# Kernel tuning notes

Measured on AMD Instinct MI355X. Metric: run time of the kernel, lower is better.

Reference implementation:

```python
import jax, jax.numpy as jnp
import numpy as np

N, C, H_IMG, W_IMG = 32, 3, 224, 224
P = 14                      # number_patches per side
PH, PW = H_IMG // P, W_IMG // P
IN_DIM = C * PH * PW        # 768
D = 768                     # hidden_dimension
NH = 12                     # number_heads
DH = D // NH                # 64
L = 12                      # number_blocks
OUT = 1000                  # output_dimension
S = P * P + 1               # 197 tokens (cls + patches)
MLP = 4 * D                 # mlp_ratio * d


def sinusoidal_pos_emb(s, d):
    # result[i][j] = sin(i / 10000^(j/d)) if j even else cos(i / 10000^((j-1)/d))
    i = np.arange(s, dtype=np.float64)[:, None]
    j = np.arange(d)[None, :]
    angle = i / (10000.0 ** ((j - (j % 2)) / float(d)))
    emb = np.where(j % 2 == 0, np.sin(angle), np.cos(angle))
    return jnp.asarray(emb, jnp.float32)


def setup_inputs() -> dict:
    key = jax.random.key(0)
    ks = jax.random.split(key, 12)
    f32 = jnp.float32
    p = {}
    p['images'] = jax.random.normal(ks[0], (N, C, H_IMG, W_IMG), f32)
    p['W_map'] = jax.random.normal(ks[1], (IN_DIM, D), f32) * 0.02
    p['b_map'] = jnp.zeros((D,), f32)
    p['class_token'] = jax.random.normal(ks[2], (1, D), f32)
    p['pos_emb'] = sinusoidal_pos_emb(S, D)  # frozen (requires_grad=False)
    p['ln1_g'] = jnp.ones((L, D), f32)
    p['ln1_b'] = jnp.zeros((L, D), f32)
    p['Wq'] = jax.random.normal(ks[3], (L, NH, DH, DH), f32) * 0.02
    p['bq'] = jnp.zeros((L, NH, DH), f32)
    p['Wk'] = jax.random.normal(ks[4], (L, NH, DH, DH), f32) * 0.02
    p['bk'] = jnp.zeros((L, NH, DH), f32)
    p['Wv'] = jax.random.normal(ks[5], (L, NH, DH, DH), f32) * 0.02
    p['bv'] = jnp.zeros((L, NH, DH), f32)
    p['ln2_g'] = jnp.ones((L, D), f32)
    p['ln2_b'] = jnp.zeros((L, D), f32)
    p['W1'] = jax.random.normal(ks[6], (L, D, MLP), f32) * 0.02
    p['b1'] = jnp.zeros((L, MLP), f32)
    p['W2'] = jax.random.normal(ks[7], (L, MLP, D), f32) * 0.02
    p['b2'] = jnp.zeros((L, D), f32)
    p['W_head'] = jax.random.normal(ks[8], (D, OUT), f32) * 0.02
    p['b_head'] = jnp.zeros((OUT,), f32)
    return p


def _layer_norm(x, g, b, eps=1e-5):
    mu = jnp.mean(x, axis=-1, keepdims=True)
    var = jnp.var(x, axis=-1, keepdims=True)
    return (x - mu) * jax.lax.rsqrt(var + eps) * g + b


def reference(images, W_map, b_map, class_token, pos_emb, ln1_g, ln1_b,
              Wq, bq, Wk, bk, Wv, bv, ln2_g, ln2_b, W1, b1, W2, b2,
              W_head, b_head):
    n = images.shape[0]
    # patchify: [N,C,H,W] -> [N, P*P, C*ph*pw]; per-patch flatten is (C,ph,pw) order
    patches = images.reshape(n, C, P, PH, P, PW)
    patches = patches.transpose(0, 2, 4, 1, 3, 5).reshape(n, P * P, IN_DIM)
    tokens = patches @ W_map + b_map                         # [N, P*P, D]
    cls = jnp.broadcast_to(class_token[None], (n, 1, D))
    x = jnp.concatenate([cls, tokens], axis=1) + pos_emb     # [N, S, D]

    scale = DH ** 0.5
    for l in range(L):
        # --- MHSA with per-head independent Linear weights ---
        h = _layer_norm(x, ln1_g[l], ln1_b[l])
        xh = h.reshape(n, S, NH, DH)
        q = jnp.einsum('nshd,hde->nshe', xh, Wq[l]) + bq[l]
        k = jnp.einsum('nshd,hde->nshe', xh, Wk[l]) + bk[l]
        v = jnp.einsum('nshd,hde->nshe', xh, Wv[l]) + bv[l]
        scores = jnp.einsum('nqhd,nkhd->nhqk', q, k) / scale  # [N,H,S,S]
        attn = jax.nn.softmax(scores, axis=-1)
        o = jnp.einsum('nhqk,nkhd->nqhd', attn, v).reshape(n, S, D)
        x = x + o
        # --- MLP (exact GELU, as torch.nn.GELU default) ---
        h2 = _layer_norm(x, ln2_g[l], ln2_b[l])
        m = jax.nn.gelu(h2 @ W1[l] + b1[l], approximate=False) @ W2[l] + b2[l]
        x = x + m

    logits = x[:, 0] @ W_head + b_head
    return jax.nn.softmax(logits, axis=-1)
```

## Files before the change

kernel.cpp:

```cpp
#include <hip/hip_runtime.h>
#include <hip/hip_bf16.h>

constexpr int N_   = 32;
constexpr int C_   = 3;
constexpr int P_   = 14;
constexpr int PHW  = 16;
constexpr int IND  = 768;
constexpr int D_   = 768;
constexpr int NH_  = 12;
constexpr int DH_  = 64;
constexpr int L_   = 12;
constexpr int OUT_ = 1000;
constexpr int S_   = 197;
constexpr int MLP_ = 3072;
constexpr int NPATCH = P_ * P_;
constexpr int ROWS   = N_ * S_;
constexpr int TROWS  = N_ * NPATCH;
constexpr int RPAD   = 6400;
constexpr int SP_R   = 256;
constexpr int SP_C   = 224;

typedef __attribute__((ext_vector_type(8))) short bf16x8;
typedef __attribute__((ext_vector_type(4))) float f32x4;

__device__ __forceinline__ float bf2f(ushort u) {
    union { float f; unsigned int i; } v; v.i = ((unsigned int)u) << 16; return v.f;
}
__device__ __forceinline__ ushort f2bf(float f) {
    union { float f; unsigned int i; } v; v.f = f;
    unsigned int r = v.i + 0x7fffu + ((v.i >> 16) & 1u);
    return (ushort)(r >> 16);
}

__global__ __launch_bounds__(256)
void mfma_gemm(const ushort* __restrict__ Ag,
               const ushort* __restrict__ Bg,
               void* __restrict__ Cg,
               const float* __restrict__ biasg,
               int M, int N, int K,
               int lda, int ldb, int ldc,
               long offA1, long offA2,
               long offB1, long offB2,
               long offC1, long offC2,
               long offS1, long offS2,
               int inner, float alpha, int act, int outbf, int accum,
               int swz, ushort* __restrict__ vtout, int splitK)
{
    const int bz = blockIdx.z;
    const int bi = bz / inner, bj = bz % inner;
    const ushort* A = Ag + bi * offA1 + bj * offA2;
    const ushort* B = Bg + bi * offB1 + bj * offB2;
    const long coff = bi * offC1 + bj * offC2;
    const float* bias = biasg ? (biasg + bi * offS1 + bj * offS2) : nullptr;

    int bx = blockIdx.x, by = blockIdx.y;
    if (swz) {
        const int gx = gridDim.x;
        const int nwg = gx * gridDim.y;
        const int orig = by * gx + bx;
        const int q = nwg >> 3, r = nwg & 7;
        const int xcd = orig & 7, loc = orig >> 3;
        const int wgid = (xcd < r ? xcd * (q + 1) : r * (q + 1) + (xcd - r) * q) + loc;
        bx = wgid % gx;
        by = wgid / gx;
    }

    __shared__ ushort As[2][128 * 32];
    __shared__ ushort Bs[2][128 * 32];

    const int tid  = threadIdx.x;
    const int w    = tid >> 6;
    const int lhi  = (tid & 63) >> 4;
    const int llo  = tid & 15;
    const int wr   = w >> 1, wc = w & 1;
    const int row0 = by * 128;
    const int col0 = bx * 128;

    f32x4 acc[4][4];
#pragma unroll
    for (int m = 0; m < 4; ++m)
#pragma unroll
        for (int n = 0; n < 4; ++n) acc[m][n] = (f32x4){0.f, 0.f, 0.f, 0.f};

    const int r0s = tid >> 2,        s0s = tid & 3;
    const int r1s = 64 + (tid >> 2), s1s = tid & 3;
    const int ss0 = s0s ^ ((r0s >> 1) & 3);
    const int ss1 = s1s ^ ((r1s >> 1) & 3);
    const int dst0 = (w << 6) << 3;
    const int dst1 = (256 + (w << 6)) << 3;

    const long arow0 = (long)(row0 + r0s) * lda + ss0 * 8;
    const long arow1 = (long)(row0 + r1s) * lda + ss1 * 8;
    const long brow0 = (long)(col0 + r0s) * ldb + ss0 * 8;
    const long brow1 = (long)(col0 + r1s) * ldb + ss1 * 8;

    const int kperblk = K / splitK;
    const int kbase   = (splitK > 1) ? bi * kperblk : 0;

#define STAGE(buf, k0)                                                                     \
    do {                                                                                   \
        __builtin_amdgcn_global_load_lds(                                                  \
            (const __attribute__((address_space(1))) void*)(A + arow0 + (k0)),             \
            (__attribute__((address_space(3))) void*)(&As[buf][0] + dst0), 16, 0, 0);      \
        __builtin_amdgcn_global_load_lds(                                                  \
            (const __attribute__((address_space(1))) void*)(A + arow1 + (k0)),             \
            (__attribute__((address_space(3))) void*)(&As[buf][0] + dst1), 16, 0, 0);      \
        __builtin_amdgcn_global_load_lds(                                                  \
            (const __attribute__((address_space(1))) void*)(B + brow0 + (k0)),             \
            (__attribute__((address_space(3))) void*)(&Bs[buf][0] + dst0), 16, 0, 0);      \
        __builtin_amdgcn_global_load_lds(                                                  \
            (const __attribute__((address_space(1))) void*)(B + brow1 + (k0)),             \
            (__attribute__((address_space(3))) void*)(&Bs[buf][0] + dst1), 16, 0, 0);      \
    } while (0)

    const int nt = kperblk >> 5;
    STAGE(0, kbase);
    for (int t = 0; t < nt; ++t) {
        const int cur = t & 1;
        if (t + 1 < nt) {
            STAGE(cur ^ 1, kbase + ((t + 1) << 5));
            asm volatile("s_waitcnt vmcnt(4)" ::: "memory");
        } else {
            asm volatile("s_waitcnt vmcnt(0)" ::: "memory");
        }
        __builtin_amdgcn_s_barrier();
        asm volatile("" ::: "memory");

        bf16x8 av[4], bv[4];
#pragma unroll
        for (int m = 0; m < 4; ++m) {
            int R = wr * 64 + m * 16 + llo;
            av[m] = *(const bf16x8*)(&As[cur][0] + R * 32 + ((lhi ^ ((R >> 1) & 3)) << 3));
        }
#pragma unroll
        for (int n = 0; n < 4; ++n) {
            int R = wc * 64 + n * 16 + llo;
            bv[n] = *(const bf16x8*)(&Bs[cur][0] + R * 32 + ((lhi ^ ((R >> 1) & 3)) << 3));
        }
#pragma unroll
        for (int m = 0; m < 4; ++m)
#pragma unroll
            for (int n = 0; n < 4; ++n)
                acc[m][n] = __builtin_amdgcn_mfma_f32_16x16x32_bf16(av[m], bv[n], acc[m][n], 0, 0, 0);

        asm volatile("" ::: "memory");
        __builtin_amdgcn_s_barrier();
    }
#undef STAGE

    float* Cf = (float*)Cg + coff;
    ushort* Ch = (ushort*)Cg + coff;
    const bool vpath = (vtout != nullptr) && (bi == 2);
#pragma unroll
    for (int m = 0; m < 4; ++m) {
#pragma unroll
        for (int n = 0; n < 4; ++n) {
#pragma unroll
            for (int j = 0; j < 4; ++j) {
                int gr = row0 + wr * 64 + m * 16 + lhi * 4 + j;
                int gc = col0 + wc * 64 + n * 16 + llo;
                if (gr >= M || gc >= N) continue;
                float v = acc[m][n][j] * alpha;
                if (splitK > 1) {
                    if (bias && bi == 0) v += bias[gc];
                    unsafeAtomicAdd(&Cf[(long)gr * ldc + gc], v);
                    continue;
                }
                if (bias) v += bias[gc];
                if (act == 1) v = 0.5f * v * (1.f + erff(v * 0.70710678118654752f));
                if (vpath) {
                    int nn = gr / 197, s = gr - nn * 197;
                    vtout[(((long)nn * NH_ + bj) * 64 + gc) * SP_C + s] = f2bf(v);
                } else {
                    long ci = (long)gr * ldc + gc;
                    if (outbf) {
                        Ch[ci] = f2bf(v);
                    } else {
                        if (accum) v += Cf[ci];
                        Cf[ci] = v;
                    }
                }
            }
        }
    }
}

__global__ __launch_bounds__(256)
void im2col_kernel(const float* __restrict__ img, ushort* __restrict__ patches)
{
    long idx = (long)blockIdx.x * 256 + threadIdx.x;
    if (idx >= (long)TROWS * IND) return;
    int e = (int)(idx % IND);
    int t = (int)((idx / IND) % NPATCH);
    int n = (int)(idx / ((long)IND * NPATCH));
    int pw = e & 15, ph = (e >> 4) & 15, c = e >> 8;
    int px = t % P_, py = t / P_;
    patches[idx] = f2bf(img[(((long)n * C_ + c) * 224 + py * PHW + ph) * 224 + px * PHW + pw]);
}

__global__ __launch_bounds__(256)
void assemble_kernel(const float* __restrict__ tokens,
                     const float* __restrict__ cls,
                     const float* __restrict__ pos,
                     float* __restrict__ x)
{
    long idx = (long)blockIdx.x * 256 + threadIdx.x;
    if (idx >= (long)ROWS * D_) return;
    int d = (int)(idx % D_);
    int s = (int)((idx / D_) % S_);
    long n = idx / ((long)D_ * S_);
    float v = (s == 0) ? cls[d] : tokens[((long)n * NPATCH + (s - 1)) * D_ + d];
    x[idx] = v + pos[(long)s * D_ + d];
}

__global__ __launch_bounds__(256)
void layernorm_kernel(const float* __restrict__ x, ushort* __restrict__ out,
                      const float* __restrict__ g, const float* __restrict__ b)
{
    long row = blockIdx.x;
    const float* xr = x + row * D_;
    ushort* orow = out + row * D_;
    int tid = threadIdx.x;
    float v0 = xr[tid], v1 = xr[tid + 256], v2 = xr[tid + 512];
    float s  = v0 + v1 + v2;
    float sq = v0 * v0 + v1 * v1 + v2 * v2;
    for (int off = 32; off > 0; off >>= 1) {
        s  += __shfl_down(s, off);
        sq += __shfl_down(sq, off);
    }
    __shared__ float rs[4], rq[4];
    int wave = tid >> 6, lane = tid & 63;
    if (lane == 0) { rs[wave] = s; rq[wave] = sq; }
    __syncthreads();
    float S  = rs[0] + rs[1] + rs[2] + rs[3];
    float SQ = rq[0] + rq[1] + rq[2] + rq[3];
    float mean = S * (1.f / 768.f);
    float var  = SQ * (1.f / 768.f) - mean * mean;
    float rstd = rsqrtf(var + 1e-5f);
    orow[tid]       = f2bf((v0 - mean) * rstd * g[tid]       + b[tid]);
    orow[tid + 256] = f2bf((v1 - mean) * rstd * g[tid + 256] + b[tid + 256]);
    orow[tid + 512] = f2bf((v2 - mean) * rstd * g[tid + 512] + b[tid + 512]);
}

__global__ __launch_bounds__(256)
void softmax197_kernel(ushort* __restrict__ scores)
{
    long rid = (long)blockIdx.x * 4 + (threadIdx.x >> 6);
    if (rid >= (long)N_ * NH_ * S_) return;
    long batch = rid / S_;
    long r = rid % S_;
    ushort* p = scores + (batch * SP_R + r) * SP_C;
    int lane = threadIdx.x & 63;
    float v[4];
    float mx = -INFINITY;
#pragma unroll
    for (int i = 0; i < 4; ++i) {
        int idx = lane + i * 64;
        v[i] = (idx < S_) ? bf2f(p[idx]) : -INFINITY;
        mx = fmaxf(mx, v[i]);
    }
    for (int off = 32; off > 0; off >>= 1) mx = fmaxf(mx, __shfl_xor(mx, off));
    float sum = 0.f;
#pragma unroll
    for (int i = 0; i < 4; ++i) {
        int idx = lane + i * 64;
        if (idx < S_) { v[i] = expf(v[i] - mx); sum += v[i]; }
    }
    for (int off = 32; off > 0; off >>= 1) sum += __shfl_xor(sum, off);
    float inv = 1.f / sum;
#pragma unroll
    for (int i = 0; i < 4; ++i) {
        int idx = lane + i * 64;
        if (idx < SP_C) p[idx] = (idx < S_) ? f2bf(v[i] * inv) : (ushort)0;
    }
}

__global__ __launch_bounds__(256)
void transcast_kernel(const float* __restrict__ in, ushort* __restrict__ out,
                      int R, int C, long inL, long outL)
{
    const float* ip = in + (long)blockIdx.z * inL;
    ushort* op = out + (long)blockIdx.z * outL;
    __shared__ float t[32][33];
    int c0 = blockIdx.x * 32, r0 = blockIdx.y * 32;
    int tx = threadIdx.x & 31, ty = threadIdx.x >> 5;
#pragma unroll
    for (int i = 0; i < 4; ++i) {
        int r = r0 + ty * 4 + i, c = c0 + tx;
        float v = 0.f;
        if (r < R && c < C) v = ip[(long)r * C + c];
        t[ty * 4 + i][tx] = v;
    }
    __syncthreads();
#pragma unroll
    for (int i = 0; i < 4; ++i) {
        int c = c0 + ty * 4 + i, r = r0 + tx;
        if (c < C && r < R) op[(long)c * R + r] = f2bf(t[tx][ty * 4 + i]);
    }
}

__global__ __launch_bounds__(256)
void transf32_kernel(const float* __restrict__ in, float* __restrict__ out, int R, int C)
{
    __shared__ float t[32][33];
    int c0 = blockIdx.x * 32, r0 = blockIdx.y * 32;
    int tx = threadIdx.x & 31, ty = threadIdx.x >> 5;
#pragma unroll
    for (int i = 0; i < 4; ++i) {
        int r = r0 + ty * 4 + i, c = c0 + tx;
        float v = 0.f;
        if (r < R && c < C) v = in[(long)r * C + c];
        t[ty * 4 + i][tx] = v;
    }
    __syncthreads();
#pragma unroll
    for (int i = 0; i < 4; ++i) {
        int c = c0 + ty * 4 + i, r = r0 + tx;
        if (c < C && r < R) out[(long)c * R + r] = t[tx][ty * 4 + i];
    }
}

__global__ __launch_bounds__(256)
void build_wqkvC_kernel(const float* __restrict__ Wq, const float* __restrict__ Wk,
                        const float* __restrict__ Wv, int l0, ushort* __restrict__ out)
{
    long idx = (long)blockIdx.x * 256 + threadIdx.x;
    if (idx >= 36L * 4096) return;
    int z = blockIdx.z, l = l0 + z;
    int sec = (int)(idx / 49152);
    int r   = (int)(idx % 49152);
    int h = r / 4096, rr = r % 4096, e = rr / 64, d = rr % 64;
    const float* W = sec == 0 ? Wq : (sec == 1 ? Wk : Wv);
    out[(long)z * 147456 + idx] = f2bf(W[(((long)l * NH_ + h) * 64 + d) * 64 + e]);
}

__global__ __launch_bounds__(256)
void build_bqkv_kernel(const float* __restrict__ bq, const float* __restrict__ bk,
                       const float* __restrict__ bv, float* __restrict__ out)
{
    int i = blockIdx.x * 256 + threadIdx.x;
    if (i >= L_ * 2304) return;
    int l = i / 2304, n = i % 2304;
    int sec = n / 768, h = (n % 768) / 64, e = n % 64;
    const float* b = sec == 0 ? bq : (sec == 1 ? bk : bv);
    out[i] = b[((long)l * NH_ + h) * 64 + e];
}

__global__ __launch_bounds__(256)
void head_kernel(const float* __restrict__ x, const float* __restrict__ Wt,
                 const float* __restrict__ bhead, float* __restrict__ logits)
{
    int wid = blockIdx.x * 4 + (threadIdx.x >> 6);
    int lane = threadIdx.x & 63;
    int n = wid / OUT_, c = wid % OUT_;
    if (n >= N_) return;
    const float* xr = x + (long)n * S_ * D_;
    const float* wr = Wt + (long)c * D_;
    float acc = 0.f;
#pragma unroll
    for (int i = 0; i < 12; ++i) acc += xr[lane + i * 64] * wr[lane + i * 64];
    for (int off = 32; off > 0; off >>= 1) acc += __shfl_down(acc, off);
    if (lane == 0) logits[(long)n * OUT_ + c] = acc + bhead[c];
}

__global__ __launch_bounds__(256)
void softmax_out_kernel(const float* __restrict__ logits, float* __restrict__ out)
{
    int row = blockIdx.x;
    int tid = threadIdx.x;
    const float* p = logits + (long)row * OUT_;
    float v[4];
    float mx = -INFINITY;
#pragma unroll
    for (int i = 0; i < 4; ++i) {
        int idx = tid + i * 256;
        v[i] = (idx < OUT_) ? p[idx] : -INFINITY;
        mx = fmaxf(mx, v[i]);
    }
    int wave = tid >> 6, lane = tid & 63;
    for (int off = 32; off > 0; off >>= 1) mx = fmaxf(mx, __shfl_xor(mx, off));
    __shared__ float r1[4], r2[4];
    if (lane == 0) r1[wave] = mx;
    __syncthreads();
    mx = fmaxf(fmaxf(r1[0], r1[1]), fmaxf(r1[2], r1[3]));
    float sum = 0.f;
#pragma unroll
    for (int i = 0; i < 4; ++i) {
        int idx = tid + i * 256;
        if (idx < OUT_) { v[i] = expf(v[i] - mx); sum += v[i]; }
    }
    for (int off = 32; off > 0; off >>= 1) sum += __shfl_xor(sum, off);
    if (lane == 0) r2[wave] = sum;
    __syncthreads();
    sum = r2[0] + r2[1] + r2[2] + r2[3];
    float inv = 1.f / sum;
#pragma unroll
    for (int i = 0; i < 4; ++i) {
        int idx = tid + i * 256;
        if (idx < OUT_) out[(long)row * OUT_ + idx] = v[i] * inv;
    }
}

extern "C" void kernel_launch(void* const* d_in, const int* in_sizes, int n_in,
                              void* d_out, int out_size, void* d_ws, size_t ws_size,
                              hipStream_t stream)
{
    const float* images = (const float*)d_in[0];
    const float* W_map  = (const float*)d_in[1];
    const float* b_map  = (const float*)d_in[2];
    const float* cls    = (const float*)d_in[3];
    const float* pos    = (const float*)d_in[4];
    const float* ln1_g  = (const float*)d_in[5];
    const float* ln1_b  = (const float*)d_in[6];
    const float* Wq     = (const float*)d_in[7];
    const float* bq     = (const float*)d_in[8];
    const float* Wk     = (const float*)d_in[9];
    const float* bk     = (const float*)d_in[10];
    const float* Wv     = (const float*)d_in[11];
    const float* bv     = (const float*)d_in[12];
    const float* ln2_g  = (const float*)d_in[13];
    const float* ln2_b  = (const float*)d_in[14];
    const float* W1     = (const float*)d_in[15];
    const float* b1     = (const float*)d_in[16];
    const float* W2     = (const float*)d_in[17];
    const float* b2     = (const float*)d_in[18];
    const float* W_head = (const float*)d_in[19];
    const float* b_head = (const float*)d_in[20];

    char* base = (char*)d_ws;
    float*  x       = (float*)base;   base += 19660800L;
    ushort* hbuf    = (ushort*)base;  base += 9830400L;
    ushort* qkv     = (ushort*)base;  base += 29491200L;
    ushort* Vt      = (ushort*)base;  base += 11038720L;
    ushort* scoresP = (ushort*)base;  base += 44040192L;
    ushort* mbuf    = (ushort*)base;  base += 39321600L;
    ushort* Wmapt   = (ushort*)base;  base += 1179648L;
    float*  bqkvA   = (float*)base;   base += 110592L;
    ushort* WqkvC   = (ushort*)base;  base += 3538944L;

    size_t used = (size_t)(base - (char*)d_ws);
    const long W1L_ALL = 56623104L, W2L_ALL = 56623104L;
    const long W1L_ONE = 4718592L,  W2L_ONE = 4718592L;
    bool hoist = ws_size >= used + (size_t)(W1L_ALL + W2L_ALL);
    ushort* W1tA = (ushort*)base;  base += hoist ? W1L_ALL : W1L_ONE;
    ushort* W2tA = (ushort*)base;  base += hoist ? W2L_ALL : W2L_ONE;
    const long w1str = hoist ? 3072L * 768 : 0;
    const long w2str = hoist ? 768L * 3072 : 0;

    float* W_headT = (float*)scoresP;
    float* logits  = (float*)((char*)scoresP + 3072000L);
    float*  tokens  = (float*)scoresP;
    ushort* patches = mbuf;

    build_wqkvC_kernel<<<dim3(576, 1, L_), 256, 0, stream>>>(Wq, Wk, Wv, 0, WqkvC);
    build_bqkv_kernel<<<(L_ * 2304 + 255) / 256, 256, 0, stream>>>(bq, bk, bv, bqkvA);
    transcast_kernel<<<dim3(24, 24, 1), 256, 0, stream>>>(W_map, Wmapt, IND, D_, 0L, 0L);
    if (hoist) {
        transcast_kernel<<<dim3(96, 24, L_), 256, 0, stream>>>(W1, W1tA, D_, MLP_,
                                                               (long)D_ * MLP_, 3072L * 768);
        transcast_kernel<<<dim3(24, 96, L_), 256, 0, stream>>>(W2, W2tA, MLP_, D_,
                                                               (long)MLP_ * D_, 768L * 3072);
    }

    {
        long tot = (long)TROWS * IND;
        im2col_kernel<<<(int)((tot + 255) / 256), 256, 0, stream>>>(images, patches);
    }
    mfma_gemm<<<dim3(D_ / 128, TROWS / 128, 1), 256, 0, stream>>>(
        patches, Wmapt, tokens, b_map,
        TROWS, D_, IND, IND, IND, D_,
        0L, 0L, 0L, 0L, 0L, 0L, 0L, 0L, 1, 1.f, 0, 0, 0, 1, nullptr, 1);
    {
        long tot = (long)ROWS * D_;
        assemble_kernel<<<(int)((tot + 255) / 256), 256, 0, stream>>>(tokens, cls, pos, x);
    }

    for (int l = 0; l < L_; ++l) {
        layernorm_kernel<<<ROWS, 256, 0, stream>>>(x, hbuf, ln1_g + (long)l * D_, ln1_b + (long)l * D_);

        mfma_gemm<<<dim3(1, RPAD / 128, 36), 256, 0, stream>>>(
            hbuf, WqkvC + (long)l * 147456, qkv, bqkvA + (long)l * 2304,
            ROWS, 64, 64, D_, 64, 2304,
            0L, 64L,
            12L * 4096, 4096L,
            768L, 64L,
            768L, 64L,
            12, 1.f, 0, 1, 0, 0, Vt, 1);

        mfma_gemm<<<dim3(2, 2, N_ * NH_), 256, 0, stream>>>(
            qkv, qkv + 768, scoresP, nullptr,
            S_, S_, DH_, 2304, 2304, SP_C,
            (long)S_ * 2304, 64L, (long)S_ * 2304, 64L,
            (long)NH_ * SP_R * SP_C, (long)SP_R * SP_C, 0L, 0L,
            NH_, 0.125f, 0, 1, 0, 0, nullptr, 1);

        softmax197_kernel<<<(N_ * NH_ * S_ + 3) / 4, 256, 0, stream>>>(scoresP);

        mfma_gemm<<<dim3(1, 2, N_ * NH_), 256, 0, stream>>>(
            scoresP, Vt, x, nullptr,
            S_, DH_, SP_C, SP_C, SP_C, D_,
            (long)NH_ * SP_R * SP_C, (long)SP_R * SP_C,
            (long)NH_ * 64 * SP_C, (long)64 * SP_C,
            (long)S_ * D_, 64L, 0L, 0L,
            NH_, 1.f, 0, 0, 1, 0, nullptr, 1);

        layernorm_kernel<<<ROWS, 256, 0, stream>>>(x, hbuf, ln2_g + (long)l * D_, ln2_b + (long)l * D_);

        if (!hoist)
            transcast_kernel<<<dim3(96, 24, 1), 256, 0, stream>>>(
                W1 + (long)l * D_ * MLP_, W1tA, D_, MLP_, 0L, 0L);
        mfma_gemm<<<dim3(MLP_ / 128, RPAD / 128, 1), 256, 0, stream>>>(
            hbuf, W1tA + (long)l * w1str, mbuf, b1 + (long)l * MLP_,
            ROWS, MLP_, D_, D_, D_, MLP_,
            0L, 0L, 0L, 0L, 0L, 0L, 0L, 0L, 1, 1.f, 1, 1, 0, 1, nullptr, 1);

        if (!hoist)
            transcast_kernel<<<dim3(24, 96, 1), 256, 0, stream>>>(
                W2 + (long)l * MLP_ * D_, W2tA, MLP_, D_, 0L, 0L);
        mfma_gemm<<<dim3(D_ / 128, RPAD / 128, 4), 256, 0, stream>>>(
            mbuf, W2tA + (long)l * w2str, x, b2 + (long)l * D_,
            ROWS, D_, MLP_, MLP_, MLP_, D_,
            0L, 0L, 0L, 0L, 0L, 0L, 0L, 0L, 1, 1.f, 0, 0, 1, 1, nullptr, 4);
    }

    transf32_kernel<<<dim3(32, 24), 256, 0, stream>>>(W_head, W_headT, D_, OUT_);
    head_kernel<<<(N_ * OUT_) / 4, 256, 0, stream>>>(x, W_headT, b_head, logits);
    softmax_out_kernel<<<N_, 256, 0, stream>>>(logits, (float*)d_out);
}
```

Measured before the change: 4.394 ms.

## Template GEMM on pipeline depth and use multi-stage LDS prefetch

```diff
diff --git a/kernel.cpp b/kernel.cpp
--- a/kernel.cpp
+++ b/kernel.cpp
@@ -32,6 +32,7 @@
     return (ushort)(r >> 16);
 }
 
+template<int R>
 __global__ __launch_bounds__(256)
 void mfma_gemm(const ushort* __restrict__ Ag,
                const ushort* __restrict__ Bg,
@@ -65,8 +66,8 @@
         by = wgid / gx;
     }
 
-    __shared__ ushort As[2][128 * 32];
-    __shared__ ushort Bs[2][128 * 32];
+    __shared__ ushort As[R][128 * 32];
+    __shared__ ushort Bs[R][128 * 32];
 
     const int tid  = threadIdx.x;
     const int w    = tid >> 6;
@@ -99,43 +100,51 @@
 
 #define STAGE(buf, k0)                                                                     \
     do {                                                                                   \
+        ushort* asb = &As[buf][0];                                                         \
+        ushort* bsb = &Bs[buf][0];                                                         \
         __builtin_amdgcn_global_load_lds(                                                  \
             (const __attribute__((address_space(1))) void*)(A + arow0 + (k0)),             \
-            (__attribute__((address_space(3))) void*)(&As[buf][0] + dst0), 16, 0, 0);      \
+            (__attribute__((address_space(3))) void*)(asb + dst0), 16, 0, 0);              \
         __builtin_amdgcn_global_load_lds(                                                  \
             (const __attribute__((address_space(1))) void*)(A + arow1 + (k0)),             \
-            (__attribute__((address_space(3))) void*)(&As[buf][0] + dst1), 16, 0, 0);      \
+            (__attribute__((address_space(3))) void*)(asb + dst1), 16, 0, 0);              \
         __builtin_amdgcn_global_load_lds(                                                  \
             (const __attribute__((address_space(1))) void*)(B + brow0 + (k0)),             \
-            (__attribute__((address_space(3))) void*)(&Bs[buf][0] + dst0), 16, 0, 0);      \
+            (__attribute__((address_space(3))) void*)(bsb + dst0), 16, 0, 0);              \
         __builtin_amdgcn_global_load_lds(                                                  \
             (const __attribute__((address_space(1))) void*)(B + brow1 + (k0)),             \
-            (__attribute__((address_space(3))) void*)(&Bs[buf][0] + dst1), 16, 0, 0);      \
+            (__attribute__((address_space(3))) void*)(bsb + dst1), 16, 0, 0);              \
     } while (0)
 
     const int nt = kperblk >> 5;
-    STAGE(0, kbase);
+#pragma unroll
+    for (int p = 0; p < R - 1; ++p)
+        if (p < nt) STAGE(p, kbase + (p << 5));
+
+    int cur = 0;
+    int stg = R - 1;
     for (int t = 0; t < nt; ++t) {
-        const int cur = t & 1;
-        if (t + 1 < nt) {
-            STAGE(cur ^ 1, kbase + ((t + 1) << 5));
-            asm volatile("s_waitcnt vmcnt(4)" ::: "memory");
-        } else {
-            asm volatile("s_waitcnt vmcnt(0)" ::: "memory");
-        }
+        const int rem = nt - 1 - t;
+        const int wv  = rem < (R - 2) ? rem : (R - 2);
+        if (wv >= 3)      asm volatile("s_waitcnt vmcnt(12)" ::: "memory");
+        else if (wv == 2) asm volatile("s_waitcnt vmcnt(8)"  ::: "memory");
+        else if (wv == 1) asm volatile("s_waitcnt vmcnt(4)"  ::: "memory");
+        else              asm volatile("s_waitcnt vmcnt(0)"  ::: "memory");
         __builtin_amdgcn_s_barrier();
         asm volatile("" ::: "memory");
 
+        if (t + R - 1 < nt) STAGE(stg, kbase + ((t + R - 1) << 5));
+
         bf16x8 av[4], bv[4];
 #pragma unroll
         for (int m = 0; m < 4; ++m) {
-            int R = wr * 64 + m * 16 + llo;
-            av[m] = *(const bf16x8*)(&As[cur][0] + R * 32 + ((lhi ^ ((R >> 1) & 3)) << 3));
+            int Rr = wr * 64 + m * 16 + llo;
+            av[m] = *(const bf16x8*)(&As[cur][0] + Rr * 32 + ((lhi ^ ((Rr >> 1) & 3)) << 3));
         }
 #pragma unroll
         for (int n = 0; n < 4; ++n) {
-            int R = wc * 64 + n * 16 + llo;
-            bv[n] = *(const bf16x8*)(&Bs[cur][0] + R * 32 + ((lhi ^ ((R >> 1) & 3)) << 3));
+            int Rr = wc * 64 + n * 16 + llo;
+            bv[n] = *(const bf16x8*)(&Bs[cur][0] + Rr * 32 + ((lhi ^ ((Rr >> 1) & 3)) << 3));
         }
 #pragma unroll
         for (int m = 0; m < 4; ++m)
@@ -143,8 +152,8 @@
             for (int n = 0; n < 4; ++n)
                 acc[m][n] = __builtin_amdgcn_mfma_f32_16x16x32_bf16(av[m], bv[n], acc[m][n], 0, 0, 0);
 
-        asm volatile("" ::: "memory");
-        __builtin_amdgcn_s_barrier();
+        if (++cur == R) cur = 0;
+        if (++stg == R) stg = 0;
     }
 #undef STAGE
 
@@ -466,7 +475,7 @@
         long tot = (long)TROWS * IND;
         im2col_kernel<<<(int)((tot + 255) / 256), 256, 0, stream>>>(images, patches);
     }
-    mfma_gemm<<<dim3(D_ / 128, TROWS / 128, 1), 256, 0, stream>>>(
+    mfma_gemm<5><<<dim3(D_ / 128, TROWS / 128, 1), 256, 0, stream>>>(
         patches, Wmapt, tokens, b_map,
         TROWS, D_, IND, IND, IND, D_,
         0L, 0L, 0L, 0L, 0L, 0L, 0L, 0L, 1, 1.f, 0, 0, 0, 1, nullptr, 1);
@@ -478,7 +487,7 @@
     for (int l = 0; l < L_; ++l) {
         layernorm_kernel<<<ROWS, 256, 0, stream>>>(x, hbuf, ln1_g + (long)l * D_, ln1_b + (long)l * D_);
 
-        mfma_gemm<<<dim3(1, RPAD / 128, 36), 256, 0, stream>>>(
+        mfma_gemm<3><<<dim3(1, RPAD / 128, 36), 256, 0, stream>>>(
             hbuf, WqkvC + (long)l * 147456, qkv, bqkvA + (long)l * 2304,
             ROWS, 64, 64, D_, 64, 2304,
             0L, 64L,
@@ -487,7 +496,7 @@
             768L, 64L,
             12, 1.f, 0, 1, 0, 0, Vt, 1);
 
-        mfma_gemm<<<dim3(2, 2, N_ * NH_), 256, 0, stream>>>(
+        mfma_gemm<3><<<dim3(2, 2, N_ * NH_), 256, 0, stream>>>(
             qkv, qkv + 768, scoresP, nullptr,
             S_, S_, DH_, 2304, 2304, SP_C,
             (long)S_ * 2304, 64L, (long)S_ * 2304, 64L,
@@ -496,7 +505,7 @@
 
         softmax197_kernel<<<(N_ * NH_ * S_ + 3) / 4, 256, 0, stream>>>(scoresP);
 
-        mfma_gemm<<<dim3(1, 2, N_ * NH_), 256, 0, stream>>>(
+        mfma_gemm<3><<<dim3(1, 2, N_ * NH_), 256, 0, stream>>>(
             scoresP, Vt, x, nullptr,
             S_, DH_, SP_C, SP_C, SP_C, D_,
             (long)NH_ * SP_R * SP_C, (long)SP_R * SP_C,
@@ -509,7 +518,7 @@
         if (!hoist)
             transcast_kernel<<<dim3(96, 24, 1), 256, 0, stream>>>(
                 W1 + (long)l * D_ * MLP_, W1tA, D_, MLP_, 0L, 0L);
-        mfma_gemm<<<dim3(MLP_ / 128, RPAD / 128, 1), 256, 0, stream>>>(
+        mfma_gemm<3><<<dim3(MLP_ / 128, RPAD / 128, 1), 256, 0, stream>>>(
             hbuf, W1tA + (long)l * w1str, mbuf, b1 + (long)l * MLP_,
             ROWS, MLP_, D_, D_, D_, MLP_,
             0L, 0L, 0L, 0L, 0L, 0L, 0L, 0L, 1, 1.f, 1, 1, 0, 1, nullptr, 1);
@@ -517,10 +526,10 @@
         if (!hoist)
             transcast_kernel<<<dim3(24, 96, 1), 256, 0, stream>>>(
                 W2 + (long)l * MLP_ * D_, W2tA, MLP_, D_, 0L, 0L);
-        mfma_gemm<<<dim3(D_ / 128, RPAD / 128, 4), 256, 0, stream>>>(
+        mfma_gemm<5><<<dim3(D_ / 128, RPAD / 128, 1), 256, 0, stream>>>(
             mbuf, W2tA + (long)l * w2str, x, b2 + (long)l * D_,
             ROWS, D_, MLP_, MLP_, MLP_, D_,
-            0L, 0L, 0L, 0L, 0L, 0L, 0L, 0L, 1, 1.f, 0, 0, 1, 1, nullptr, 4);
+            0L, 0L, 0L, 0L, 0L, 0L, 0L, 0L, 1, 1.f, 0, 0, 1, 1, nullptr, 1);
     }
 
     transf32_kernel<<<dim3(32, 24), 256, 0, stream>>>(W_head, W_headT, D_, OUT_);
```

Measured after the change: 4.760 ms. 8.3% more time.
